# Kernel optimization log

Measured on AMD Instinct MI355X. Metric: run time of the kernel, lower is better.

Reference implementation:

```python
import jax, jax.numpy as jnp
import numpy as np

B, H, T, D = 2, 16, 2048, 64
R1, R2 = 4, 8


def setup_inputs() -> dict:
    key = jax.random.key(0)
    ks = jax.random.split(key, 7)
    return {
        "q": jax.random.normal(ks[0], (B, H, T, D), dtype=jnp.float32),
        "k": jax.random.normal(ks[1], (B, H, T, D), dtype=jnp.float32),
        "v": jax.random.normal(ks[2], (B, H, T, D), dtype=jnp.float32),
        "W_q": jax.random.normal(ks[3], (H, D, R1 * R2), dtype=jnp.float32) / np.sqrt(D),
        "W_k": jax.random.normal(ks[4], (H, D, R1 * R2), dtype=jnp.float32) / np.sqrt(D),
        "core1": jax.random.normal(ks[5], (H, R1), dtype=jnp.float32),
        "core2": jax.random.normal(ks[6], (H, R2), dtype=jnp.float32),
    }


def reference(q, k, v, W_q, W_k, core1, core2):
    """Kronecker low-rank (LSR) causal attention.

    scores[b,h,m,n] = (1/sqrt(R1*R2)) * sum_r kron[h,r] * (q@W_q)[b,h,m,r] * (k@W_k)[b,h,n,r]
    where kron[h] = core1[h] (x) core2[h]  (per-head Kronecker product).
    """
    Hh, r1 = core1.shape
    r2 = core2.shape[1]
    # per-head Kronecker core vector: (H, R1*R2)
    kron = (core1[:, :, None] * core2[:, None, :]).reshape(Hh, r1 * r2)
    scale = 1.0 / jnp.sqrt(jnp.float32(r1 * r2))
    # low-rank projections, rank R = R1*R2
    q_lr = jnp.einsum("bhtd,hdr->bhtr", q, W_q) * kron[None, :, None, :]  # [B,H,T,R]
    k_lr = jnp.einsum("bhtd,hdr->bhtr", k, W_k)                            # [B,H,T,R]
    scores = jnp.einsum("bhmr,bhnr->bhmn", q_lr, k_lr) * scale             # [B,H,T,T]
    t = q.shape[2]
    causal = jnp.tril(jnp.ones((t, t), dtype=bool))
    scores = jnp.where(causal[None, None], scores, -jnp.inf)
    p = jax.nn.softmax(scores, axis=-1)
    return jnp.einsum("bhmn,bhnd->bhmd", p, v)
```

## Files before the change

### kernel.cpp

```cpp
#include <hip/hip_runtime.h>

typedef _Float16 f16;
typedef _Float16 f16x2 __attribute__((ext_vector_type(2)));
typedef _Float16 f16x4 __attribute__((ext_vector_type(4)));
typedef _Float16 f16x8 __attribute__((ext_vector_type(8)));
typedef float    f32x4 __attribute__((ext_vector_type(4)));

constexpr int B_ = 2, H_ = 16, T_ = 2048, D_ = 64, R_ = 32, NT = 32;
constexpr int NROW = B_ * H_ * T_;

__device__ __forceinline__ f32x4 mfma16(f16x8 a, f16x8 b, f32x4 c) {
  return __builtin_amdgcn_mfma_f32_16x16x32_f16(a, b, c, 0, 0, 0);
}
__device__ __forceinline__ void ld_lds16(const void* g, void* l) {
  __builtin_amdgcn_global_load_lds(
      (const __attribute__((address_space(1))) unsigned int*)g,
      (__attribute__((address_space(3))) unsigned int*)l, 16, 0, 0);
}

__global__ __launch_bounds__(256) void proj_kernel(
    const float* __restrict__ q, const float* __restrict__ k, const float* __restrict__ v,
    const float* __restrict__ Wq, const float* __restrict__ Wk,
    const float* __restrict__ c1, const float* __restrict__ c2,
    f16* __restrict__ qlr, f16* __restrict__ klr, f16* __restrict__ vt)
{
  __shared__ float sv[64 * 65];
  __shared__ __align__(16) f16 s_w[2][32 * 64];
  __shared__ __align__(16) f16 s_qk[2][64 * 32];

  const int tid = threadIdx.x, w = tid >> 6, lane = tid & 63;
  const int l15 = lane & 15, l4 = lane >> 4;
  const int bh = blockIdx.x >> 5, h = bh & (H_ - 1);
  const int t0 = (blockIdx.x & 31) * 64;

  const float* vb = v + ((size_t)bh * T_ + t0) * D_;
  float4 vld[4];
#pragma unroll
  for (int it = 0; it < 4; ++it) vld[it] = ((const float4*)vb)[it * 256 + tid];

  const int m = t0 + 16 * w + l15;
  const float* qr = q + ((size_t)bh * T_ + m) * D_;
  const float* kr = k + ((size_t)bh * T_ + m) * D_;
  f16x8 aq[2], ak[2];
#pragma unroll
  for (int kc = 0; kc < 2; ++kc) {
    float4 x0 = *(const float4*)(qr + kc * 32 + 8 * l4);
    float4 x1 = *(const float4*)(qr + kc * 32 + 8 * l4 + 4);
    float4 y0 = *(const float4*)(kr + kc * 32 + 8 * l4);
    float4 y1 = *(const float4*)(kr + kc * 32 + 8 * l4 + 4);
    f16x8 A, K;
    A[0]=(f16)x0.x; A[1]=(f16)x0.y; A[2]=(f16)x0.z; A[3]=(f16)x0.w;
    A[4]=(f16)x1.x; A[5]=(f16)x1.y; A[6]=(f16)x1.z; A[7]=(f16)x1.w;
    K[0]=(f16)y0.x; K[1]=(f16)y0.y; K[2]=(f16)y0.z; K[3]=(f16)y0.w;
    K[4]=(f16)y1.x; K[5]=(f16)y1.y; K[6]=(f16)y1.z; K[7]=(f16)y1.w;
    aq[kc] = A; ak[kc] = K;
  }

  const float* Wqh = Wq + (size_t)h * D_ * R_;
  const float* Wkh = Wk + (size_t)h * D_ * R_;
#pragma unroll
  for (int mm = 0; mm < 2; ++mm) {
    const float* Wh = mm ? Wkh : Wqh;
#pragma unroll
    for (int it = 0; it < 2; ++it) {
      const int flat = it * 1024 + tid * 4;
      const int d = flat >> 5, r = flat & 31;
      const float4 wv = *(const float4*)(Wh + flat);
#pragma unroll
      for (int e = 0; e < 4; ++e) {
        const int rr = r + e;
        s_w[mm][rr * 64 + ((((d >> 3) ^ (rr & 7)) << 3) | (d & 7))] = (f16)((&wv.x)[e]);
      }
    }
  }

#pragma unroll
  for (int it = 0; it < 4; ++it) {
    const int i4 = it * 256 + tid, t = i4 >> 4, dq = (i4 & 15) * 4;
    sv[t * 65 + dq    ] = vld[it].x;
    sv[t * 65 + dq + 1] = vld[it].y;
    sv[t * 65 + dq + 2] = vld[it].z;
    sv[t * 65 + dq + 3] = vld[it].w;
  }

  __syncthreads();

  f16x8 bq[2][2], bk[2][2];
#pragma unroll
  for (int kc = 0; kc < 2; ++kc)
#pragma unroll
    for (int nt = 0; nt < 2; ++nt) {
      const int r = 16 * nt + l15;
      const int d0 = kc * 32 + 8 * l4;
      const int idx = r * 64 + (((d0 >> 3) ^ (r & 7)) << 3);
      bq[kc][nt] = *(const f16x8*)&s_w[0][idx];
      bk[kc][nt] = *(const f16x8*)&s_w[1][idx];
    }

  const f32x4 z4 = {0.f, 0.f, 0.f, 0.f};
#pragma unroll
  for (int nt = 0; nt < 2; ++nt) {
    f32x4 accq = mfma16(aq[0], bq[0][nt], z4);
    accq = mfma16(aq[1], bq[1][nt], accq);
    f32x4 acck = mfma16(ak[0], bk[0][nt], z4);
    acck = mfma16(ak[1], bk[1][nt], acck);
    const int r = 16 * nt + l15;
    const float scl = c1[h * 4 + (r >> 3)] * c2[h * 8 + (r & 7)] *
                      (0.17677669529663687f * 1.4426950408889634f);
#pragma unroll
    for (int i = 0; i < 4; ++i) {
      const int lrow = 16 * w + 4 * l4 + i;
      s_qk[0][lrow * 32 + r] = (f16)(accq[i] * scl);
      s_qk[1][lrow * 32 + r] = (f16)acck[i];
    }
  }

#pragma unroll
  for (int it = 0; it < 8; ++it) {
    const int idx = it * 256 + tid, d = idx >> 5, t = (idx & 31) * 2;
    const float f0 = sv[t * 65 + d], f1 = sv[t * 65 + 65 + d];
    f16x2 pr; pr[0] = (f16)f0; pr[1] = (f16)f1;
    const int sw = ((((t >> 3) ^ (d & 7)) << 3) | (t & 7));
    *(f16x2*)(vt + ((size_t)bh * D_ + d) * T_ + t0 + sw) = pr;
  }

  __syncthreads();

  const int lrow = tid >> 2;
  const int r0 = (tid & 3) * 8;
  const f16x8 vq = *(const f16x8*)&s_qk[0][lrow * 32 + r0];
  *(f16x8*)(qlr + ((size_t)bh * T_ + t0 + lrow) * R_ + r0) = vq;
  const f16x8 vk = *(const f16x8*)&s_qk[1][lrow * 32 + r0];
  *(f16x8*)(klr + ((size_t)bh * T_ + t0 + lrow) * R_ + r0) = vk;
}

__global__ __launch_bounds__(256) void attn_kernel(
    const f16* __restrict__ qlr, const f16* __restrict__ klr,
    const f16* __restrict__ vt, f16* __restrict__ On, float2* __restrict__ ml,
    const int NS)
{
  __shared__ __align__(16) f16 s_k[64 * 32];
  __shared__ __align__(16) f16 s_vt[64 * 64];
  __shared__ __align__(16) f16 s_p[4][16 * 64];

  const int tid = threadIdx.x, w = tid >> 6, lane = tid & 63;
  const int l15 = lane & 15, l4 = lane >> 4;
  const int bh = blockIdx.x & 31;
  const int rest = blockIdx.x >> 5;
  const int nsl = (NS == 4) ? 2 : (NS == 2) ? 1 : 0;
  const int mt = 31 - (rest >> nsl);
  const int s  = rest & (NS - 1);
  const int m0 = mt * 64;

  const f16x8 aq = *(const f16x8*)(qlr + ((size_t)bh * T_ + m0 + 16 * w + l15) * R_ + 8 * l4);

  const f16* kb = klr + (size_t)bh * T_ * R_;
  const f16* vb = vt + (size_t)bh * D_ * T_;

  const f32x4 z4 = {0.f, 0.f, 0.f, 0.f};
  f32x4 oacc[4];
#pragma unroll
  for (int d = 0; d < 4; ++d) oacc[d] = z4;
  float mi = -1e30f, li = 0.f;

  for (int j = s; j <= mt; j += NS) {
    const int n0 = 64 * j;
    __syncthreads();
    ld_lds16((const char*)kb + (size_t)n0 * 64 + w * 1024 + lane * 16,
             (char*)s_k + w * 1024);
#pragma unroll
    for (int e = 0; e < 2; ++e) {
      const int d0 = 16 * w + e * 8;
      ld_lds16((const char*)vb + ((size_t)(d0 + (lane >> 3)) * T_ + n0) * 2 + (lane & 7) * 16,
               (char*)s_vt + d0 * 128);
    }
    __syncthreads();

    f32x4 sc[4];
#pragma unroll
    for (int ns = 0; ns < 4; ++ns) {
      f16x8 akf = *(const f16x8*)&s_k[(16 * ns + l15) * 32 + 8 * l4];
      sc[ns] = mfma16(akf, aq, z4);
    }
    if (j == mt) {
      const int lim = 16 * w + l15;
#pragma unroll
      for (int ns = 0; ns < 4; ++ns) {
        const int nb = 16 * ns + 4 * l4;
#pragma unroll
        for (int i = 0; i < 4; ++i)
          if (nb + i > lim) sc[ns][i] = -1e30f;
      }
    }

    float rm = -1e30f;
#pragma unroll
    for (int ns = 0; ns < 4; ++ns)
#pragma unroll
      for (int i = 0; i < 4; ++i) rm = fmaxf(rm, sc[ns][i]);
    rm = fmaxf(rm, __shfl_xor(rm, 16));
    rm = fmaxf(rm, __shfl_xor(rm, 32));
    const float mn = fmaxf(mi, rm);
    const float a = exp2f(mi - mn);
    float rs = 0.f;
#pragma unroll
    for (int ns = 0; ns < 4; ++ns) {
      f16x4 pf;
#pragma unroll
      for (int i = 0; i < 4; ++i) {
        const float p = exp2f(sc[ns][i] - mn);
        rs += p; pf[i] = (f16)p;
      }
      const int col = ((((2 * ns + (l4 >> 1)) ^ (l15 & 7)) << 3) | (4 * (l4 & 1)));
      *(f16x4*)&s_p[w][l15 * 64 + col] = pf;
    }
    rs += __shfl_xor(rs, 16);
    rs += __shfl_xor(rs, 32);
    li = li * a + rs; mi = mn;
#pragma unroll
    for (int d = 0; d < 4; ++d) oacc[d] *= a;

#pragma unroll
    for (int nk = 0; nk < 2; ++nk) {
      const int u = (4 * nk + l4) ^ (l15 & 7);
      f16x8 bp = *(const f16x8*)&s_p[w][l15 * 64 + u * 8];
#pragma unroll
      for (int dblk = 0; dblk < 4; ++dblk) {
        f16x8 av = *(const f16x8*)&s_vt[(16 * dblk + l15) * 64 + u * 8];
        oacc[dblk] = mfma16(av, bp, oacc[dblk]);
      }
    }
  }

  const float invl = li > 0.f ? 1.f / li : 0.f;
  f16* ob = On + (((size_t)s * 32 + bh) * T_ + m0 + 16 * w + l15) * D_;
#pragma unroll
  for (int dblk = 0; dblk < 4; ++dblk) {
    f16x4 o;
#pragma unroll
    for (int i = 0; i < 4; ++i) o[i] = (f16)(oacc[dblk][i] * invl);
    *(f16x4*)(ob + 16 * dblk + 4 * l4) = o;
  }
  if (l4 == 0) {
    float2 mlv; mlv.x = mi; mlv.y = li;
    ml[((size_t)s * 32 + bh) * T_ + m0 + 16 * w + l15] = mlv;
  }
}

__global__ __launch_bounds__(256) void merge_kernel(
    const f16* __restrict__ On, const float2* __restrict__ ml,
    float* __restrict__ out, const int NS)
{
  const int row = blockIdx.x * 32 + (threadIdx.x >> 3);
  const int d0 = (threadIdx.x & 7) * 8;
  float res[8];
  if (NS == 4) {
    const float2 a0 = ml[row];
    const float2 a1 = ml[1 * NROW + row];
    const float2 a2 = ml[2 * NROW + row];
    const float2 a3 = ml[3 * NROW + row];
    const f16x8 o0 = *(const f16x8*)(On + (size_t)row * 64 + d0);
    const f16x8 o1 = *(const f16x8*)(On + ((size_t)1 * NROW + row) * 64 + d0);
    const f16x8 o2 = *(const f16x8*)(On + ((size_t)2 * NROW + row) * 64 + d0);
    const f16x8 o3 = *(const f16x8*)(On + ((size_t)3 * NROW + row) * 64 + d0);
    const float ms = fmaxf(fmaxf(a0.x, a1.x), fmaxf(a2.x, a3.x));
    const float w0 = exp2f(a0.x - ms) * a0.y;
    const float w1 = exp2f(a1.x - ms) * a1.y;
    const float w2 = exp2f(a2.x - ms) * a2.y;
    const float w3 = exp2f(a3.x - ms) * a3.y;
    const float inv = 1.f / (w0 + w1 + w2 + w3);
    const float c0 = w0 * inv, c1 = w1 * inv, c2 = w2 * inv, c3 = w3 * inv;
#pragma unroll
    for (int e = 0; e < 8; ++e)
      res[e] = c0 * (float)o0[e] + c1 * (float)o1[e] + c2 * (float)o2[e] + c3 * (float)o3[e];
  } else if (NS == 2) {
    const float2 a = ml[row];
    const float2 b = ml[NROW + row];
    const f16x8 o0 = *(const f16x8*)(On + (size_t)row * 64 + d0);
    const f16x8 o1 = *(const f16x8*)(On + ((size_t)NROW + row) * 64 + d0);
    const float ms = fmaxf(a.x, b.x);
    const float w0 = exp2f(a.x - ms) * a.y;
    const float w1 = exp2f(b.x - ms) * b.y;
    const float inv = 1.f / (w0 + w1);
    const float c0 = w0 * inv, c1 = w1 * inv;
#pragma unroll
    for (int e = 0; e < 8; ++e) res[e] = c0 * (float)o0[e] + c1 * (float)o1[e];
  } else {
    const f16x8 o0 = *(const f16x8*)(On + (size_t)row * 64 + d0);
#pragma unroll
    for (int e = 0; e < 8; ++e) res[e] = (float)o0[e];
  }
  float* ob = out + (size_t)row * 64 + d0;
  f32x4 r0, r1;
#pragma unroll
  for (int e = 0; e < 4; ++e) { r0[e] = res[e]; r1[e] = res[4 + e]; }
  *(f32x4*)ob = r0;
  *(f32x4*)(ob + 4) = r1;
}

extern "C" void kernel_launch(void* const* d_in, const int* in_sizes, int n_in,
                              void* d_out, int out_size, void* d_ws, size_t ws_size,
                              hipStream_t stream) {
  const float* q  = (const float*)d_in[0];
  const float* k  = (const float*)d_in[1];
  const float* v  = (const float*)d_in[2];
  const float* Wq = (const float*)d_in[3];
  const float* Wk = (const float*)d_in[4];
  const float* c1 = (const float*)d_in[5];
  const float* c2 = (const float*)d_in[6];
  float* out = (float*)d_out;

  const size_t MB = 1 << 20;
  int NS = 1;
  if (ws_size >= 16 * MB + 4 * (8 * MB + NROW * sizeof(float2))) NS = 4;
  else if (ws_size >= 16 * MB + 2 * (8 * MB + NROW * sizeof(float2))) NS = 2;

  f16* qlr = (f16*)d_ws;
  f16* klr = qlr + (size_t)B_ * H_ * T_ * R_;
  f16* vt  = klr + (size_t)B_ * H_ * T_ * R_;
  f16* On  = vt + (size_t)B_ * H_ * T_ * D_;
  float2* ml = (float2*)(On + (size_t)NS * NROW * D_);

  proj_kernel<<<B_ * H_ * NT, 256, 0, stream>>>(q, k, v, Wq, Wk, c1, c2, qlr, klr, vt);
  attn_kernel<<<B_ * H_ * NT * NS, 256, 0, stream>>>(qlr, klr, vt, On, ml, NS);
  merge_kernel<<<NROW / 32, 256, 0, stream>>>(On, ml, out, NS);
}
```

Measured before the change: 145.6 us.

## Drop split-KV partitioning and merge kernel; write fp32 output directly

Removes the split-KV scheme, where each query tile's key range was split into NS strided partitions, along with the separate merge kernel that combined partial outputs using their max/sum statistics. Each block now processes its full causal key range and writes normalized fp32 output straight to the result. This saves a kernel launch, the fp16 partial-output writes, and the merge pass's reads. In exchange it cuts grid parallelism by up to 4x (1024 blocks instead of 4096) and leaves long serial loops for the late query tiles, which may leave the GPU underutilized.

```diff
diff --git a/kernel.cpp b/kernel.cpp
--- a/kernel.cpp
+++ b/kernel.cpp
@@ -136,8 +136,7 @@
 
 __global__ __launch_bounds__(256) void attn_kernel(
     const f16* __restrict__ qlr, const f16* __restrict__ klr,
-    const f16* __restrict__ vt, f16* __restrict__ On, float2* __restrict__ ml,
-    const int NS)
+    const f16* __restrict__ vt, float* __restrict__ out)
 {
   __shared__ __align__(16) f16 s_k[64 * 32];
   __shared__ __align__(16) f16 s_vt[64 * 64];
@@ -146,10 +145,7 @@
   const int tid = threadIdx.x, w = tid >> 6, lane = tid & 63;
   const int l15 = lane & 15, l4 = lane >> 4;
   const int bh = blockIdx.x & 31;
-  const int rest = blockIdx.x >> 5;
-  const int nsl = (NS == 4) ? 2 : (NS == 2) ? 1 : 0;
-  const int mt = 31 - (rest >> nsl);
-  const int s  = rest & (NS - 1);
+  const int mt = 31 - (blockIdx.x >> 5);
   const int m0 = mt * 64;
 
   const f16x8 aq = *(const f16x8*)(qlr + ((size_t)bh * T_ + m0 + 16 * w + l15) * R_ + 8 * l4);
@@ -163,7 +159,7 @@
   for (int d = 0; d < 4; ++d) oacc[d] = z4;
   float mi = -1e30f, li = 0.f;
 
-  for (int j = s; j <= mt; j += NS) {
+  for (int j = 0; j <= mt; ++j) {
     const int n0 = 64 * j;
     __syncthreads();
     ld_lds16((const char*)kb + (size_t)n0 * 64 + w * 1024 + lane * 16,
@@ -233,69 +229,14 @@
   }
 
   const float invl = li > 0.f ? 1.f / li : 0.f;
-  f16* ob = On + (((size_t)s * 32 + bh) * T_ + m0 + 16 * w + l15) * D_;
+  float* ob = out + ((size_t)bh * T_ + m0 + 16 * w + l15) * D_;
 #pragma unroll
   for (int dblk = 0; dblk < 4; ++dblk) {
-    f16x4 o;
-#pragma unroll
-    for (int i = 0; i < 4; ++i) o[i] = (f16)(oacc[dblk][i] * invl);
-    *(f16x4*)(ob + 16 * dblk + 4 * l4) = o;
-  }
-  if (l4 == 0) {
-    float2 mlv; mlv.x = mi; mlv.y = li;
-    ml[((size_t)s * 32 + bh) * T_ + m0 + 16 * w + l15] = mlv;
-  }
-}
-
-__global__ __launch_bounds__(256) void merge_kernel(
-    const f16* __restrict__ On, const float2* __restrict__ ml,
-    float* __restrict__ out, const int NS)
-{
-  const int row = blockIdx.x * 32 + (threadIdx.x >> 3);
-  const int d0 = (threadIdx.x & 7) * 8;
-  float res[8];
-  if (NS == 4) {
-    const float2 a0 = ml[row];
-    const float2 a1 = ml[1 * NROW + row];
-    const float2 a2 = ml[2 * NROW + row];
-    const float2 a3 = ml[3 * NROW + row];
-    const f16x8 o0 = *(const f16x8*)(On + (size_t)row * 64 + d0);
-    const f16x8 o1 = *(const f16x8*)(On + ((size_t)1 * NROW + row) * 64 + d0);
-    const f16x8 o2 = *(const f16x8*)(On + ((size_t)2 * NROW + row) * 64 + d0);
-    const f16x8 o3 = *(const f16x8*)(On + ((size_t)3 * NROW + row) * 64 + d0);
-    const float ms = fmaxf(fmaxf(a0.x, a1.x), fmaxf(a2.x, a3.x));
-    const float w0 = exp2f(a0.x - ms) * a0.y;
-    const float w1 = exp2f(a1.x - ms) * a1.y;
-    const float w2 = exp2f(a2.x - ms) * a2.y;
-    const float w3 = exp2f(a3.x - ms) * a3.y;
-    const float inv = 1.f / (w0 + w1 + w2 + w3);
-    const float c0 = w0 * inv, c1 = w1 * inv, c2 = w2 * inv, c3 = w3 * inv;
-#pragma unroll
-    for (int e = 0; e < 8; ++e)
-      res[e] = c0 * (float)o0[e] + c1 * (float)o1[e] + c2 * (float)o2[e] + c3 * (float)o3[e];
-  } else if (NS == 2) {
-    const float2 a = ml[row];
-    const float2 b = ml[NROW + row];
-    const f16x8 o0 = *(const f16x8*)(On + (size_t)row * 64 + d0);
-    const f16x8 o1 = *(const f16x8*)(On + ((size_t)NROW + row) * 64 + d0);
-    const float ms = fmaxf(a.x, b.x);
-    const float w0 = exp2f(a.x - ms) * a.y;
-    const float w1 = exp2f(b.x - ms) * b.y;
-    const float inv = 1.f / (w0 + w1);
-    const float c0 = w0 * inv, c1 = w1 * inv;
-#pragma unroll
-    for (int e = 0; e < 8; ++e) res[e] = c0 * (float)o0[e] + c1 * (float)o1[e];
-  } else {
-    const f16x8 o0 = *(const f16x8*)(On + (size_t)row * 64 + d0);
-#pragma unroll
-    for (int e = 0; e < 8; ++e) res[e] = (float)o0[e];
-  }
-  float* ob = out + (size_t)row * 64 + d0;
-  f32x4 r0, r1;
-#pragma unroll
-  for (int e = 0; e < 4; ++e) { r0[e] = res[e]; r1[e] = res[4 + e]; }
-  *(f32x4*)ob = r0;
-  *(f32x4*)(ob + 4) = r1;
+    f32x4 o;
+#pragma unroll
+    for (int i = 0; i < 4; ++i) o[i] = oacc[dblk][i] * invl;
+    *(f32x4*)(ob + 16 * dblk + 4 * l4) = o;
+  }
 }
 
 extern "C" void kernel_launch(void* const* d_in, const int* in_sizes, int n_in,
@@ -310,18 +251,10 @@
   const float* c2 = (const float*)d_in[6];
   float* out = (float*)d_out;
 
-  const size_t MB = 1 << 20;
-  int NS = 1;
-  if (ws_size >= 16 * MB + 4 * (8 * MB + NROW * sizeof(float2))) NS = 4;
-  else if (ws_size >= 16 * MB + 2 * (8 * MB + NROW * sizeof(float2))) NS = 2;
-
   f16* qlr = (f16*)d_ws;
   f16* klr = qlr + (size_t)B_ * H_ * T_ * R_;
   f16* vt  = klr + (size_t)B_ * H_ * T_ * R_;
-  f16* On  = vt + (size_t)B_ * H_ * T_ * D_;
-  float2* ml = (float2*)(On + (size_t)NS * NROW * D_);
 
   proj_kernel<<<B_ * H_ * NT, 256, 0, stream>>>(q, k, v, Wq, Wk, c1, c2, qlr, klr, vt);
-  attn_kernel<<<B_ * H_ * NT * NS, 256, 0, stream>>>(qlr, klr, vt, On, ml, NS);
-  merge_kernel<<<NROW / 32, 256, 0, stream>>>(On, ml, out, NS);
-}
+  attn_kernel<<<B_ * H_ * NT, 256, 0, stream>>>(qlr, klr, vt, out);
+}
```

New measurement: 141.8 us. -2.6%, faster.
